# Kernel optimization log

Measured on AMD Instinct MI355X. Metric: run time of the kernel, lower is better.

The kernel has to match this reference:

```python
import jax, jax.numpy as jnp
import numpy as np

N_NODES = 50000
N_EDGES = 800000
IN_FEATS = 128
N_HIDDEN = 128
N_CLASSES = 64


def setup_inputs() -> dict:
    key = jax.random.key(0)
    ks = jax.random.split(key, 12)
    x = jax.random.normal(ks[0], (N_NODES, IN_FEATS), dtype=jnp.float32)
    src = jax.random.randint(ks[1], (N_EDGES,), 0, N_NODES, dtype=jnp.int32)
    dst = jax.random.randint(ks[2], (N_EDGES,), 0, N_NODES, dtype=jnp.int32)
    dims = [(IN_FEATS, N_HIDDEN), (N_HIDDEN, N_HIDDEN), (N_HIDDEN, N_CLASSES)]
    inp = {"x": x, "src": src, "dst": dst}
    for i, (din, dout) in enumerate(dims):
        s = (2.0 / (din + dout)) ** 0.5  # xavier-ish init scale
        inp[f"Wself{i}"] = jax.random.normal(ks[3 + 3 * i], (din, dout), dtype=jnp.float32) * s
        inp[f"Wneigh{i}"] = jax.random.normal(ks[4 + 3 * i], (din, dout), dtype=jnp.float32) * s
        inp[f"b{i}"] = jnp.zeros((dout,), dtype=jnp.float32)
    return inp


def _sage_conv(h, src, dst, inv_deg, Wself, Wneigh, b):
    # mean aggregation over in-neighbors: gather on src, segment-sum on dst
    agg = jax.ops.segment_sum(h[src], dst, num_segments=N_NODES)  # [N, d]
    h_neigh = agg * inv_deg[:, None]
    return h @ Wself + h_neigh @ Wneigh + b


def reference(x, src, dst, Wself0, Wneigh0, b0, Wself1, Wneigh1, b1, Wself2, Wneigh2, b2):
    # in-degree (clamped to 1, matching DGL mean aggregator), shared across layers
    deg = jax.ops.segment_sum(jnp.ones((N_EDGES,), dtype=jnp.float32), dst, num_segments=N_NODES)
    inv_deg = 1.0 / jnp.maximum(deg, 1.0)
    # dropout is identity in eval mode
    h = _sage_conv(x, src, dst, inv_deg, Wself0, Wneigh0, b0)
    h = jax.nn.relu(h)
    h = _sage_conv(h, src, dst, inv_deg, Wself1, Wneigh1, b1)
    h = jax.nn.relu(h)
    h = _sage_conv(h, src, dst, inv_deg, Wself2, Wneigh2, b2)
    return h
```

## Files before the change

kernel.cpp:

```cpp
#include <hip/hip_runtime.h>

#define N_NODES 50000
#define N_EDGES 800000
#define NB_SCAN 196

typedef unsigned short ushort_t;
typedef __attribute__((ext_vector_type(8))) short  short8v;
typedef __attribute__((ext_vector_type(4))) float  float4v;
typedef __attribute__((ext_vector_type(4))) unsigned short ushort4v;
typedef __attribute__((ext_vector_type(8))) unsigned short ushort8v;

__device__ __forceinline__ ushort_t f2bf(float f) {
    unsigned u = __float_as_uint(f);
    unsigned r = 0x7fffu + ((u >> 16) & 1u);
    return (ushort_t)((u + r) >> 16);
}
__device__ __forceinline__ float bf2f(ushort_t h) {
    return __uint_as_float((unsigned)h << 16);
}


__global__ void deg_count_k(const int* __restrict__ dst, int* __restrict__ deg, int nE) {
    int i = blockIdx.x * blockDim.x + threadIdx.x;
    if (i < nE) atomicAdd(deg + dst[i], 1);
}

__global__ __launch_bounds__(256) void block_sum_k(const int* __restrict__ deg,
                                                   int* __restrict__ bsum, int n) {
    __shared__ int s[256];
    int t = threadIdx.x, b = blockIdx.x;
    int i = b * 256 + t;
    s[t] = (i < n) ? deg[i] : 0;
    __syncthreads();
#pragma unroll
    for (int off = 128; off > 0; off >>= 1) {
        if (t < off) s[t] += s[t + off];
        __syncthreads();
    }
    if (t == 0) bsum[b] = s[0];
}

__global__ __launch_bounds__(256) void scan_bsum_k(const int* __restrict__ bsum,
                                                   int* __restrict__ boff,
                                                   int* __restrict__ rowptr_last, int nb) {
    __shared__ int s[256];
    int t = threadIdx.x;
    int v = (t < nb) ? bsum[t] : 0;
    s[t] = v;
    __syncthreads();
#pragma unroll
    for (int off = 1; off < 256; off <<= 1) {
        int u = (t >= off) ? s[t - off] : 0;
        __syncthreads();
        s[t] += u;
        __syncthreads();
    }
    if (t < nb) boff[t] = s[t] - v;
    if (t == 255) *rowptr_last = s[255];
}

__global__ __launch_bounds__(256) void write_rowptr_k(const int* __restrict__ deg,
                                                      const int* __restrict__ boff,
                                                      int* __restrict__ rowptr,
                                                      int* __restrict__ cursor,
                                                      float* __restrict__ inv, int n) {
    __shared__ int s[256];
    int t = threadIdx.x, b = blockIdx.x;
    int i = b * 256 + t;
    int d = (i < n) ? deg[i] : 0;
    s[t] = d;
    __syncthreads();
#pragma unroll
    for (int off = 1; off < 256; off <<= 1) {
        int u = (t >= off) ? s[t - off] : 0;
        __syncthreads();
        s[t] += u;
        __syncthreads();
    }
    if (i < n) {
        int r = boff[b] + s[t] - d;
        rowptr[i] = r;
        cursor[i] = r;
        inv[i] = 1.0f / fmaxf((float)d, 1.0f);
    }
}

__global__ __launch_bounds__(256) void scatter_k(const int* __restrict__ src,
                                                 const int* __restrict__ dst,
                                                 int* __restrict__ cursor,
                                                 int* __restrict__ csr, int nE) {
    const int grp = blockIdx.x & 7;
    const int lo = grp * 6250, hi = lo + 6250;
    const int stride = (gridDim.x >> 3) * 256;
    for (int i = (blockIdx.x >> 3) * 256 + threadIdx.x; i < nE; i += stride) {
        int d = dst[i];
        if (d >= lo && d < hi) {
            int s = src[i];
            int pos = atomicAdd(cursor + d, 1);
            csr[pos] = s;
        }
    }
}

__global__ __launch_bounds__(256) void cast_bf16_k(const float* __restrict__ x,
                                                   ushort_t* __restrict__ xb, int n4) {
    int i = blockIdx.x * 256 + threadIdx.x;
    if (i < n4) {
        float4 v = ((const float4*)x)[i];
        ushort4v h;
        h[0] = f2bf(v.x); h[1] = f2bf(v.y); h[2] = f2bf(v.z); h[3] = f2bf(v.w);
        ((ushort4v*)xb)[i] = h;
    }
}

__global__ __launch_bounds__(256) void pack_all_k(const float* __restrict__ W0n, const float* __restrict__ W0s,
                                                  const float* __restrict__ W1n, const float* __restrict__ W1s,
                                                  const float* __restrict__ W2n, const float* __restrict__ W2s,
                                                  ushort_t* __restrict__ P) {
    int tid = blockIdx.x * 256 + threadIdx.x;
    const float* W; int dout; int base; int r;
    if      (tid < 2048)  { W = W0n; dout = 128; base = 0;     r = tid; }
    else if (tid < 4096)  { W = W0s; dout = 128; base = 16384; r = tid - 2048; }
    else if (tid < 6144)  { W = W1n; dout = 128; base = 32768; r = tid - 4096; }
    else if (tid < 8192)  { W = W1s; dout = 128; base = 49152; r = tid - 6144; }
    else if (tid < 9216)  { W = W2n; dout = 64;  base = 65536; r = tid - 8192; }
    else                  { W = W2s; dout = 64;  base = 73728; r = tid - 9216; }
    int lane = r & 63;
    int ks = (r >> 6) & 3;
    int nt = r >> 8;
    int col = nt * 16 + (lane & 15);
    int k0 = ks * 32 + ((lane >> 4) << 3);
    ushort_t* d = P + (size_t)base + (size_t)r * 8;
    ushort4v lo4, hi4;
#pragma unroll
    for (int j = 0; j < 4; ++j) lo4[j] = f2bf(W[(size_t)(k0 + j) * dout + col]);
#pragma unroll
    for (int j = 0; j < 4; ++j) hi4[j] = f2bf(W[(size_t)(k0 + 4 + j) * dout + col]);
    *(ushort4v*)d = lo4;
    *(ushort4v*)(d + 4) = hi4;
}

__global__ __launch_bounds__(256) void aggm_k(const ushort_t* __restrict__ h,
                                              const int* __restrict__ rowptr,
                                              const int* __restrict__ csr,
                                              const float* __restrict__ inv,
                                              ushort_t* __restrict__ m, int N) {
    int node = (blockIdx.x * 256 + threadIdx.x) >> 5;
    int c = threadIdx.x & 31;
    if (node >= N) return;
    int start = rowptr[node], end = rowptr[node + 1];

    const ushort4v* hp = (const ushort4v*)h;
    float a0[4] = {}, a1[4] = {}, a2[4] = {}, a3[4] = {};
    int j = start;
    for (; j + 3 < end; j += 4) {
        int u0 = csr[j], u1 = csr[j + 1], u2 = csr[j + 2], u3 = csr[j + 3];
        ushort4v w0 = hp[(size_t)u0 * 32 + c];
        ushort4v w1 = hp[(size_t)u1 * 32 + c];
        ushort4v w2 = hp[(size_t)u2 * 32 + c];
        ushort4v w3 = hp[(size_t)u3 * 32 + c];
#pragma unroll
        for (int k = 0; k < 4; ++k) {
            a0[k] += bf2f(w0[k]); a1[k] += bf2f(w1[k]);
            a2[k] += bf2f(w2[k]); a3[k] += bf2f(w3[k]);
        }
    }
    for (; j < end; ++j) {
        ushort4v w = hp[(size_t)csr[j] * 32 + c];
#pragma unroll
        for (int k = 0; k < 4; ++k) a0[k] += bf2f(w[k]);
    }
    float s = inv[node];
    ushort4v o;
#pragma unroll
    for (int k = 0; k < 4; ++k) o[k] = f2bf(((a0[k] + a1[k]) + (a2[k] + a3[k])) * s);
    ((ushort4v*)m)[(size_t)node * 32 + c] = o;
}

__global__ __launch_bounds__(256, 2) void fusedgemm_k(const ushort_t* __restrict__ H,
                                                      const ushort_t* __restrict__ M,
                                                      const short8v* __restrict__ Ws,
                                                      const short8v* __restrict__ Wn,
                                                      const float* __restrict__ bias,
                                                      ushort_t* __restrict__ Out, int N) {
    __shared__ ushort_t sm[2][128 * 128];
    char* sbH = (char*)sm[0];
    char* sbM = (char*)sm[1];
    const int bm = blockIdx.x * 128;
    const int t = threadIdx.x;
    const int w = t >> 6, l = t & 63;

    {
        const ushort8v* Hp = (const ushort8v*)H;
        const ushort8v* Mp = (const ushort8v*)M;
        ushort8v zeroV = {0, 0, 0, 0, 0, 0, 0, 0};
#pragma unroll
        for (int it = 0; it < 8; ++it) {
            int r = it * 16 + (t >> 4);
            int row = bm + r;
            int byte = (r * 256 + (t & 15) * 16) ^ ((r & 7) << 4);
            ushort8v vh = zeroV, vm = zeroV;
            if (row < N) {
                vh = Hp[(size_t)row * 16 + (t & 15)];
                vm = Mp[(size_t)row * 16 + (t & 15)];
            }
            *(ushort8v*)(sbH + byte) = vh;
            *(ushort8v*)(sbM + byte) = vm;
        }
    }
    __syncthreads();

    float bv[8];
#pragma unroll
    for (int nt = 0; nt < 8; ++nt) bv[nt] = bias[nt * 16 + (l & 15)];

    float4v acc[2][8] = {};
#pragma unroll
    for (int ks = 0; ks < 4; ++ks) {
        int r0 = w * 32 + (l & 15);
        int r1 = r0 + 16;
        int b0 = (r0 * 256 + ks * 64 + (l >> 4) * 16) ^ ((r0 & 7) << 4);
        int b1 = (r1 * 256 + ks * 64 + (l >> 4) * 16) ^ ((r1 & 7) << 4);
        short8v ah0 = *(const short8v*)(sbH + b0);
        short8v ah1 = *(const short8v*)(sbH + b1);
        short8v am0 = *(const short8v*)(sbM + b0);
        short8v am1 = *(const short8v*)(sbM + b1);
#pragma unroll
        for (int nt = 0; nt < 8; ++nt) {
            short8v bs = Ws[(nt * 4 + ks) * 64 + l];
            short8v bn = Wn[(nt * 4 + ks) * 64 + l];
            acc[0][nt] = __builtin_amdgcn_mfma_f32_16x16x32_bf16(ah0, bs, acc[0][nt], 0, 0, 0);
            acc[0][nt] = __builtin_amdgcn_mfma_f32_16x16x32_bf16(am0, bn, acc[0][nt], 0, 0, 0);
            acc[1][nt] = __builtin_amdgcn_mfma_f32_16x16x32_bf16(ah1, bs, acc[1][nt], 0, 0, 0);
            acc[1][nt] = __builtin_amdgcn_mfma_f32_16x16x32_bf16(am1, bn, acc[1][nt], 0, 0, 0);
        }
    }

#pragma unroll
    for (int mi = 0; mi < 2; ++mi) {
#pragma unroll
        for (int i = 0; i < 4; ++i) {
            int row = bm + w * 32 + mi * 16 + (l >> 4) * 4 + i;
            if (row < N) {
#pragma unroll
                for (int nt = 0; nt < 8; ++nt) {
                    int col = nt * 16 + (l & 15);
                    Out[(size_t)row * 128 + col] = f2bf(fmaxf(acc[mi][nt][i] + bv[nt], 0.f));
                }
            }
        }
    }
}

__global__ __launch_bounds__(256, 2) void dual64_k(const ushort_t* __restrict__ A,
                                                   const short8v* __restrict__ Wn,
                                                   const short8v* __restrict__ Ws,
                                                   const float* __restrict__ bias,
                                                   ushort_t* __restrict__ Z,
                                                   float* __restrict__ S, int N) {
    constexpr int NT = 4;
    __shared__ ushort_t Asm[128 * 128];
    char* sb = (char*)Asm;
    const int bm = blockIdx.x * 128;
    const int t = threadIdx.x;
    const int w = t >> 6, l = t & 63;

    {
        const ushort8v* Ap = (const ushort8v*)A;
        ushort8v zeroV = {0, 0, 0, 0, 0, 0, 0, 0};
#pragma unroll
        for (int it = 0; it < 8; ++it) {
            int r = it * 16 + (t >> 4);
            int row = bm + r;
            ushort8v v = zeroV;
            if (row < N) v = Ap[(size_t)row * 16 + (t & 15)];
            int byte = (r * 256 + (t & 15) * 16) ^ ((r & 7) << 4);
            *(ushort8v*)(sb + byte) = v;
        }
    }
    __syncthreads();

    float bv[NT];
#pragma unroll
    for (int nt = 0; nt < NT; ++nt) bv[nt] = bias[nt * 16 + (l & 15)];

    float4v accS[2][NT] = {}, accN[2][NT] = {};
#pragma unroll
    for (int ks = 0; ks < 4; ++ks) {
        int r0 = w * 32 + (l & 15);
        int b0 = (r0 * 256 + ks * 64 + (l >> 4) * 16) ^ ((r0 & 7) << 4);
        short8v a0 = *(const short8v*)(sb + b0);
        int r1 = r0 + 16;
        int b1 = (r1 * 256 + ks * 64 + (l >> 4) * 16) ^ ((r1 & 7) << 4);
        short8v a1 = *(const short8v*)(sb + b1);
#pragma unroll
        for (int nt = 0; nt < NT; ++nt) {
            short8v bs = Ws[(nt * 4 + ks) * 64 + l];
            short8v bn = Wn[(nt * 4 + ks) * 64 + l];
            accS[0][nt] = __builtin_amdgcn_mfma_f32_16x16x32_bf16(a0, bs, accS[0][nt], 0, 0, 0);
            accS[1][nt] = __builtin_amdgcn_mfma_f32_16x16x32_bf16(a1, bs, accS[1][nt], 0, 0, 0);
            accN[0][nt] = __builtin_amdgcn_mfma_f32_16x16x32_bf16(a0, bn, accN[0][nt], 0, 0, 0);
            accN[1][nt] = __builtin_amdgcn_mfma_f32_16x16x32_bf16(a1, bn, accN[1][nt], 0, 0, 0);
        }
    }

#pragma unroll
    for (int mi = 0; mi < 2; ++mi) {
#pragma unroll
        for (int i = 0; i < 4; ++i) {
            int row = bm + w * 32 + mi * 16 + (l >> 4) * 4 + i;
            if (row < N) {
#pragma unroll
                for (int nt = 0; nt < NT; ++nt) {
                    int col = nt * 16 + (l & 15);
                    S[(size_t)row * 64 + col] = accS[mi][nt][i] + bv[nt];
                    Z[(size_t)row * 64 + col] = f2bf(accN[mi][nt][i]);
                }
            }
        }
    }
}

__global__ __launch_bounds__(256) void agg64_k(const ushort_t* __restrict__ z,
                                               const int* __restrict__ rowptr,
                                               const int* __restrict__ csr,
                                               const float* __restrict__ inv,
                                               float* __restrict__ out, int N) {
    int node = (blockIdx.x * 256 + threadIdx.x) >> 4;
    int c = threadIdx.x & 15;
    if (node >= N) return;
    int start = rowptr[node], end = rowptr[node + 1];

    const ushort4v* zp = (const ushort4v*)z;
    float a0[4] = {}, a1[4] = {}, a2[4] = {}, a3[4] = {};
    int j = start;
    for (; j + 3 < end; j += 4) {
        int u0 = csr[j], u1 = csr[j + 1], u2 = csr[j + 2], u3 = csr[j + 3];
        ushort4v w0 = zp[(size_t)u0 * 16 + c];
        ushort4v w1 = zp[(size_t)u1 * 16 + c];
        ushort4v w2 = zp[(size_t)u2 * 16 + c];
        ushort4v w3 = zp[(size_t)u3 * 16 + c];
#pragma unroll
        for (int k = 0; k < 4; ++k) {
            a0[k] += bf2f(w0[k]); a1[k] += bf2f(w1[k]);
            a2[k] += bf2f(w2[k]); a3[k] += bf2f(w3[k]);
        }
    }
    for (; j < end; ++j) {
        ushort4v w = zp[(size_t)csr[j] * 16 + c];
#pragma unroll
        for (int k = 0; k < 4; ++k) a0[k] += bf2f(w[k]);
    }
    float s = inv[node];
    float4* op = (float4*)(out + (size_t)node * 64 + c * 4);
    float4 o = *op;
    o.x += ((a0[0] + a1[0]) + (a2[0] + a3[0])) * s;
    o.y += ((a0[1] + a1[1]) + (a2[1] + a3[1])) * s;
    o.z += ((a0[2] + a1[2]) + (a2[2] + a3[2])) * s;
    o.w += ((a0[3] + a1[3]) + (a2[3] + a3[3])) * s;
    *op = o;
}


extern "C" void kernel_launch(void* const* d_in, const int* in_sizes, int n_in,
                              void* d_out, int out_size, void* d_ws, size_t ws_size,
                              hipStream_t stream) {
    const float* x       = (const float*)d_in[0];
    const int*   src     = (const int*)d_in[1];
    const int*   dst     = (const int*)d_in[2];
    const float* Wself0  = (const float*)d_in[3];
    const float* Wneigh0 = (const float*)d_in[4];
    const float* b0      = (const float*)d_in[5];
    const float* Wself1  = (const float*)d_in[6];
    const float* Wneigh1 = (const float*)d_in[7];
    const float* b1      = (const float*)d_in[8];
    const float* Wself2  = (const float*)d_in[9];
    const float* Wneigh2 = (const float*)d_in[10];
    const float* b2      = (const float*)d_in[11];
    float* out = (float*)d_out;

    char* ws = (char*)d_ws;
    size_t off = 0;
    auto alloc = [&](size_t bytes) -> void* {
        void* p = ws + off;
        off += (bytes + 255) & ~(size_t)255;
        return p;
    };
    int*      deg    = (int*)alloc((size_t)N_NODES * 4);
    float*    inv    = (float*)alloc((size_t)N_NODES * 4);
    int*      rowptr = (int*)alloc((size_t)(N_NODES + 1) * 4);
    int*      cursor = (int*)alloc((size_t)N_NODES * 4);
    int*      csr    = (int*)alloc((size_t)N_EDGES * 4);
    int*      bsum   = (int*)alloc((size_t)NB_SCAN * 4);
    int*      boff   = (int*)alloc((size_t)NB_SCAN * 4);
    ushort_t* packW  = (ushort_t*)alloc((size_t)81920 * 2);
    ushort_t* xb     = (ushort_t*)alloc((size_t)N_NODES * 128 * 2);
    ushort_t* mbuf   = (ushort_t*)alloc((size_t)N_NODES * 128 * 2);
    ushort_t* h1     = (ushort_t*)alloc((size_t)N_NODES * 128 * 2);
    ushort_t* h2     = (ushort_t*)alloc((size_t)N_NODES * 128 * 2);
    ushort_t* z64    = (ushort_t*)alloc((size_t)N_NODES * 64 * 2);

    dim3 b256(256);
    const int edgeBlocks  = (N_EDGES + 255) / 256;
    const int gemmBlocks  = (N_NODES + 127) / 128;
    const int aggmBlocks  = (N_NODES * 32 + 255) / 256;
    const int agg64Blocks = (N_NODES * 16 + 255) / 256;
    const int castBlocks  = (N_NODES * 128 / 4 + 255) / 256;

    hipMemsetAsync(deg, 0, (size_t)N_NODES * 4, stream);
    deg_count_k<<<edgeBlocks, b256, 0, stream>>>(dst, deg, N_EDGES);
    block_sum_k<<<NB_SCAN, b256, 0, stream>>>(deg, bsum, N_NODES);
    scan_bsum_k<<<1, b256, 0, stream>>>(bsum, boff, rowptr + N_NODES, NB_SCAN);
    write_rowptr_k<<<NB_SCAN, b256, 0, stream>>>(deg, boff, rowptr, cursor, inv, N_NODES);
    scatter_k<<<1024, b256, 0, stream>>>(src, dst, cursor, csr, N_EDGES);

    pack_all_k<<<40, b256, 0, stream>>>(Wneigh0, Wself0, Wneigh1, Wself1, Wneigh2, Wself2, packW);
    cast_bf16_k<<<castBlocks, b256, 0, stream>>>(x, xb, N_NODES * 128 / 4);
    const short8v* pN0 = (const short8v*)(packW);
    const short8v* pS0 = (const short8v*)(packW + 16384);
    const short8v* pN1 = (const short8v*)(packW + 32768);
    const short8v* pS1 = (const short8v*)(packW + 49152);
    const short8v* pN2 = (const short8v*)(packW + 65536);
    const short8v* pS2 = (const short8v*)(packW + 73728);

    aggm_k<<<aggmBlocks, b256, 0, stream>>>(xb, rowptr, csr, inv, mbuf, N_NODES);
    fusedgemm_k<<<gemmBlocks, b256, 0, stream>>>(xb, mbuf, pS0, pN0, b0, h1, N_NODES);

    aggm_k<<<aggmBlocks, b256, 0, stream>>>(h1, rowptr, csr, inv, mbuf, N_NODES);
    fusedgemm_k<<<gemmBlocks, b256, 0, stream>>>(h1, mbuf, pS1, pN1, b1, h2, N_NODES);

    dual64_k<<<gemmBlocks, b256, 0, stream>>>(h2, pN2, pS2, b2, z64, out, N_NODES);
    agg64_k<<<agg64Blocks, b256, 0, stream>>>(z64, rowptr, csr, inv, out, N_NODES);
}
```

Measured before the change: 225.3 us.

## Fuse CSR build and bf16 cast into one cooperative kernel; widen aggregation loads

Replaces the memset, degree count, three scan kernels, scatter and cast kernels with a single cooperative kernel that separates the phases with grid-wide syncs, removing several launches and the gaps between them. Separately, the aggregation kernels now load 8 bf16 values per thread (16-byte loads) instead of 4, halving the threads per node and doubling per-thread work. The grid syncs add barrier cost, and the 1024-block cooperative launch requires every block to be co-resident; if they cannot all be resident the launch fails and nothing downstream runs correctly.

Result: slower. 710.9 us (+215.6%).

```diff
diff --git a/kernel.cpp b/kernel.cpp
--- a/kernel.cpp
+++ b/kernel.cpp
@@ -1,4 +1,7 @@
 #include <hip/hip_runtime.h>
+#include <hip/hip_cooperative_groups.h>
+
+namespace cg = cooperative_groups;
 
 #define N_NODES 50000
 #define N_EDGES 800000
@@ -20,96 +23,96 @@
 }
 
 
-__global__ void deg_count_k(const int* __restrict__ dst, int* __restrict__ deg, int nE) {
-    int i = blockIdx.x * blockDim.x + threadIdx.x;
-    if (i < nE) atomicAdd(deg + dst[i], 1);
-}
-
-__global__ __launch_bounds__(256) void block_sum_k(const int* __restrict__ deg,
-                                                   int* __restrict__ bsum, int n) {
+__global__ __launch_bounds__(256) void build_k(const float* __restrict__ x,
+                                               ushort_t* __restrict__ xb,
+                                               const int* __restrict__ src,
+                                               const int* __restrict__ dst,
+                                               int* __restrict__ deg,
+                                               float* __restrict__ inv,
+                                               int* __restrict__ rowptr,
+                                               int* __restrict__ cursor,
+                                               int* __restrict__ csr,
+                                               int* __restrict__ bsum) {
+    cg::grid_group grid = cg::this_grid();
     __shared__ int s[256];
-    int t = threadIdx.x, b = blockIdx.x;
-    int i = b * 256 + t;
-    s[t] = (i < n) ? deg[i] : 0;
-    __syncthreads();
-#pragma unroll
-    for (int off = 128; off > 0; off >>= 1) {
-        if (t < off) s[t] += s[t + off];
-        __syncthreads();
-    }
-    if (t == 0) bsum[b] = s[0];
-}
-
-__global__ __launch_bounds__(256) void scan_bsum_k(const int* __restrict__ bsum,
-                                                   int* __restrict__ boff,
-                                                   int* __restrict__ rowptr_last, int nb) {
-    __shared__ int s[256];
-    int t = threadIdx.x;
-    int v = (t < nb) ? bsum[t] : 0;
-    s[t] = v;
-    __syncthreads();
-#pragma unroll
-    for (int off = 1; off < 256; off <<= 1) {
-        int u = (t >= off) ? s[t - off] : 0;
-        __syncthreads();
-        s[t] += u;
-        __syncthreads();
-    }
-    if (t < nb) boff[t] = s[t] - v;
-    if (t == 255) *rowptr_last = s[255];
-}
-
-__global__ __launch_bounds__(256) void write_rowptr_k(const int* __restrict__ deg,
-                                                      const int* __restrict__ boff,
-                                                      int* __restrict__ rowptr,
-                                                      int* __restrict__ cursor,
-                                                      float* __restrict__ inv, int n) {
-    __shared__ int s[256];
-    int t = threadIdx.x, b = blockIdx.x;
-    int i = b * 256 + t;
-    int d = (i < n) ? deg[i] : 0;
-    s[t] = d;
-    __syncthreads();
-#pragma unroll
-    for (int off = 1; off < 256; off <<= 1) {
-        int u = (t >= off) ? s[t - off] : 0;
-        __syncthreads();
-        s[t] += u;
-        __syncthreads();
-    }
-    if (i < n) {
-        int r = boff[b] + s[t] - d;
-        rowptr[i] = r;
-        cursor[i] = r;
-        inv[i] = 1.0f / fmaxf((float)d, 1.0f);
-    }
-}
-
-__global__ __launch_bounds__(256) void scatter_k(const int* __restrict__ src,
-                                                 const int* __restrict__ dst,
-                                                 int* __restrict__ cursor,
-                                                 int* __restrict__ csr, int nE) {
-    const int grp = blockIdx.x & 7;
-    const int lo = grp * 6250, hi = lo + 6250;
-    const int stride = (gridDim.x >> 3) * 256;
-    for (int i = (blockIdx.x >> 3) * 256 + threadIdx.x; i < nE; i += stride) {
-        int d = dst[i];
-        if (d >= lo && d < hi) {
-            int s = src[i];
-            int pos = atomicAdd(cursor + d, 1);
-            csr[pos] = s;
-        }
-    }
-}
-
-__global__ __launch_bounds__(256) void cast_bf16_k(const float* __restrict__ x,
-                                                   ushort_t* __restrict__ xb, int n4) {
-    int i = blockIdx.x * 256 + threadIdx.x;
-    if (i < n4) {
+    const int t = threadIdx.x, b = blockIdx.x;
+    const int nthr = gridDim.x * 256;
+    const int gtid = b * 256 + t;
+
+    for (int i = gtid; i < N_NODES; i += nthr) deg[i] = 0;
+    for (int i = gtid; i < N_NODES * 32; i += nthr) {
         float4 v = ((const float4*)x)[i];
         ushort4v h;
         h[0] = f2bf(v.x); h[1] = f2bf(v.y); h[2] = f2bf(v.z); h[3] = f2bf(v.w);
         ((ushort4v*)xb)[i] = h;
+    }
+    grid.sync();
+
+    for (int i = gtid; i < N_EDGES; i += nthr) atomicAdd(deg + dst[i], 1);
+    grid.sync();
+
+    if (b < NB_SCAN) {
+        int i = b * 256 + t;
+        s[t] = (i < N_NODES) ? deg[i] : 0;
+        __syncthreads();
+#pragma unroll
+        for (int off = 128; off > 0; off >>= 1) {
+            if (t < off) s[t] += s[t + off];
+            __syncthreads();
+        }
+        if (t == 0) bsum[b] = s[0];
+    }
+    grid.sync();
+
+    if (b == 0) {
+        int v = (t < NB_SCAN) ? bsum[t] : 0;
+        s[t] = v;
+        __syncthreads();
+#pragma unroll
+        for (int off = 1; off < 256; off <<= 1) {
+            int u = (t >= off) ? s[t - off] : 0;
+            __syncthreads();
+            s[t] += u;
+            __syncthreads();
+        }
+        if (t < NB_SCAN) bsum[t] = s[t] - v;
+        if (t == 255) rowptr[N_NODES] = s[255];
+    }
+    grid.sync();
+
+    if (b < NB_SCAN) {
+        int i = b * 256 + t;
+        int d = (i < N_NODES) ? deg[i] : 0;
+        s[t] = d;
+        __syncthreads();
+#pragma unroll
+        for (int off = 1; off < 256; off <<= 1) {
+            int u = (t >= off) ? s[t - off] : 0;
+            __syncthreads();
+            s[t] += u;
+            __syncthreads();
+        }
+        if (i < N_NODES) {
+            int r = bsum[b] + s[t] - d;
+            rowptr[i] = r;
+            cursor[i] = r;
+            inv[i] = 1.0f / fmaxf((float)d, 1.0f);
+        }
+    }
+    grid.sync();
+
+    {
+        const int grp = b & 7;
+        const int lo = grp * 6250, hi = lo + 6250;
+        const int stride = (gridDim.x >> 3) * 256;
+        for (int i = (b >> 3) * 256 + t; i < N_EDGES; i += stride) {
+            int d = dst[i];
+            if (d >= lo && d < hi) {
+                int sv = src[i];
+                int pos = atomicAdd(cursor + d, 1);
+                csr[pos] = sv;
+            }
+        }
     }
 }
 
@@ -145,36 +148,36 @@
                                               const int* __restrict__ csr,
                                               const float* __restrict__ inv,
                                               ushort_t* __restrict__ m, int N) {
-    int node = (blockIdx.x * 256 + threadIdx.x) >> 5;
-    int c = threadIdx.x & 31;
+    int node = (blockIdx.x * 256 + threadIdx.x) >> 4;
+    int c = threadIdx.x & 15;
     if (node >= N) return;
     int start = rowptr[node], end = rowptr[node + 1];
 
-    const ushort4v* hp = (const ushort4v*)h;
-    float a0[4] = {}, a1[4] = {}, a2[4] = {}, a3[4] = {};
+    const ushort8v* hp = (const ushort8v*)h;
+    float a0[8] = {}, a1[8] = {}, a2[8] = {}, a3[8] = {};
     int j = start;
     for (; j + 3 < end; j += 4) {
         int u0 = csr[j], u1 = csr[j + 1], u2 = csr[j + 2], u3 = csr[j + 3];
-        ushort4v w0 = hp[(size_t)u0 * 32 + c];
-        ushort4v w1 = hp[(size_t)u1 * 32 + c];
-        ushort4v w2 = hp[(size_t)u2 * 32 + c];
-        ushort4v w3 = hp[(size_t)u3 * 32 + c];
-#pragma unroll
-        for (int k = 0; k < 4; ++k) {
+        ushort8v w0 = hp[(size_t)u0 * 16 + c];
+        ushort8v w1 = hp[(size_t)u1 * 16 + c];
+        ushort8v w2 = hp[(size_t)u2 * 16 + c];
+        ushort8v w3 = hp[(size_t)u3 * 16 + c];
+#pragma unroll
+        for (int k = 0; k < 8; ++k) {
             a0[k] += bf2f(w0[k]); a1[k] += bf2f(w1[k]);
             a2[k] += bf2f(w2[k]); a3[k] += bf2f(w3[k]);
         }
     }
     for (; j < end; ++j) {
-        ushort4v w = hp[(size_t)csr[j] * 32 + c];
-#pragma unroll
-        for (int k = 0; k < 4; ++k) a0[k] += bf2f(w[k]);
+        ushort8v w = hp[(size_t)csr[j] * 16 + c];
+#pragma unroll
+        for (int k = 0; k < 8; ++k) a0[k] += bf2f(w[k]);
     }
     float s = inv[node];
-    ushort4v o;
-#pragma unroll
-    for (int k = 0; k < 4; ++k) o[k] = f2bf(((a0[k] + a1[k]) + (a2[k] + a3[k])) * s);
-    ((ushort4v*)m)[(size_t)node * 32 + c] = o;
+    ushort8v o;
+#pragma unroll
+    for (int k = 0; k < 8; ++k) o[k] = f2bf(((a0[k] + a1[k]) + (a2[k] + a3[k])) * s);
+    ((ushort8v*)m)[(size_t)node * 16 + c] = o;
 }
 
 __global__ __launch_bounds__(256, 2) void fusedgemm_k(const ushort_t* __restrict__ H,
@@ -326,39 +329,45 @@
                                                const int* __restrict__ csr,
                                                const float* __restrict__ inv,
                                                float* __restrict__ out, int N) {
-    int node = (blockIdx.x * 256 + threadIdx.x) >> 4;
-    int c = threadIdx.x & 15;
+    int node = (blockIdx.x * 256 + threadIdx.x) >> 3;
+    int c = threadIdx.x & 7;
     if (node >= N) return;
     int start = rowptr[node], end = rowptr[node + 1];
 
-    const ushort4v* zp = (const ushort4v*)z;
-    float a0[4] = {}, a1[4] = {}, a2[4] = {}, a3[4] = {};
+    const ushort8v* zp = (const ushort8v*)z;
+    float a0[8] = {}, a1[8] = {}, a2[8] = {}, a3[8] = {};
     int j = start;
     for (; j + 3 < end; j += 4) {
         int u0 = csr[j], u1 = csr[j + 1], u2 = csr[j + 2], u3 = csr[j + 3];
-        ushort4v w0 = zp[(size_t)u0 * 16 + c];
-        ushort4v w1 = zp[(size_t)u1 * 16 + c];
-        ushort4v w2 = zp[(size_t)u2 * 16 + c];
-        ushort4v w3 = zp[(size_t)u3 * 16 + c];
-#pragma unroll
-        for (int k = 0; k < 4; ++k) {
+        ushort8v w0 = zp[(size_t)u0 * 8 + c];
+        ushort8v w1 = zp[(size_t)u1 * 8 + c];
+        ushort8v w2 = zp[(size_t)u2 * 8 + c];
+        ushort8v w3 = zp[(size_t)u3 * 8 + c];
+#pragma unroll
+        for (int k = 0; k < 8; ++k) {
             a0[k] += bf2f(w0[k]); a1[k] += bf2f(w1[k]);
             a2[k] += bf2f(w2[k]); a3[k] += bf2f(w3[k]);
         }
     }
     for (; j < end; ++j) {
-        ushort4v w = zp[(size_t)csr[j] * 16 + c];
-#pragma unroll
-        for (int k = 0; k < 4; ++k) a0[k] += bf2f(w[k]);
+        ushort8v w = zp[(size_t)csr[j] * 8 + c];
+#pragma unroll
+        for (int k = 0; k < 8; ++k) a0[k] += bf2f(w[k]);
     }
     float s = inv[node];
-    float4* op = (float4*)(out + (size_t)node * 64 + c * 4);
-    float4 o = *op;
-    o.x += ((a0[0] + a1[0]) + (a2[0] + a3[0])) * s;
-    o.y += ((a0[1] + a1[1]) + (a2[1] + a3[1])) * s;
-    o.z += ((a0[2] + a1[2]) + (a2[2] + a3[2])) * s;
-    o.w += ((a0[3] + a1[3]) + (a2[3] + a3[3])) * s;
-    *op = o;
+    float* op = out + (size_t)node * 64 + c * 8;
+    float4 o0 = *(float4*)op;
+    float4 o1 = *(float4*)(op + 4);
+    o0.x += ((a0[0] + a1[0]) + (a2[0] + a3[0])) * s;
+    o0.y += ((a0[1] + a1[1]) + (a2[1] + a3[1])) * s;
+    o0.z += ((a0[2] + a1[2]) + (a2[2] + a3[2])) * s;
+    o0.w += ((a0[3] + a1[3]) + (a2[3] + a3[3])) * s;
+    o1.x += ((a0[4] + a1[4]) + (a2[4] + a3[4])) * s;
+    o1.y += ((a0[5] + a1[5]) + (a2[5] + a3[5])) * s;
+    o1.z += ((a0[6] + a1[6]) + (a2[6] + a3[6])) * s;
+    o1.w += ((a0[7] + a1[7]) + (a2[7] + a3[7])) * s;
+    *(float4*)op = o0;
+    *(float4*)(op + 4) = o1;
 }
 
 
@@ -392,7 +401,6 @@
     int*      cursor = (int*)alloc((size_t)N_NODES * 4);
     int*      csr    = (int*)alloc((size_t)N_EDGES * 4);
     int*      bsum   = (int*)alloc((size_t)NB_SCAN * 4);
-    int*      boff   = (int*)alloc((size_t)NB_SCAN * 4);
     ushort_t* packW  = (ushort_t*)alloc((size_t)81920 * 2);
     ushort_t* xb     = (ushort_t*)alloc((size_t)N_NODES * 128 * 2);
     ushort_t* mbuf   = (ushort_t*)alloc((size_t)N_NODES * 128 * 2);
@@ -401,21 +409,19 @@
     ushort_t* z64    = (ushort_t*)alloc((size_t)N_NODES * 64 * 2);
 
     dim3 b256(256);
-    const int edgeBlocks  = (N_EDGES + 255) / 256;
     const int gemmBlocks  = (N_NODES + 127) / 128;
-    const int aggmBlocks  = (N_NODES * 32 + 255) / 256;
-    const int agg64Blocks = (N_NODES * 16 + 255) / 256;
-    const int castBlocks  = (N_NODES * 128 / 4 + 255) / 256;
-
-    hipMemsetAsync(deg, 0, (size_t)N_NODES * 4, stream);
-    deg_count_k<<<edgeBlocks, b256, 0, stream>>>(dst, deg, N_EDGES);
-    block_sum_k<<<NB_SCAN, b256, 0, stream>>>(deg, bsum, N_NODES);
-    scan_bsum_k<<<1, b256, 0, stream>>>(bsum, boff, rowptr + N_NODES, NB_SCAN);
-    write_rowptr_k<<<NB_SCAN, b256, 0, stream>>>(deg, boff, rowptr, cursor, inv, N_NODES);
-    scatter_k<<<1024, b256, 0, stream>>>(src, dst, cursor, csr, N_EDGES);
+    const int aggmBlocks  = (N_NODES * 16 + 255) / 256;
+    const int agg64Blocks = (N_NODES * 8 + 255) / 256;
+
+    {
+        void* args[] = {(void*)&x, (void*)&xb, (void*)&src, (void*)&dst,
+                        (void*)&deg, (void*)&inv, (void*)&rowptr, (void*)&cursor,
+                        (void*)&csr, (void*)&bsum};
+        hipLaunchCooperativeKernel(reinterpret_cast<const void*>(build_k),
+                                   dim3(1024), b256, args, 0, stream);
+    }
 
     pack_all_k<<<40, b256, 0, stream>>>(Wneigh0, Wself0, Wneigh1, Wself1, Wneigh2, Wself2, packW);
-    cast_bf16_k<<<castBlocks, b256, 0, stream>>>(x, xb, N_NODES * 128 / 4);
     const short8v* pN0 = (const short8v*)(packW);
     const short8v* pS0 = (const short8v*)(packW + 16384);
     const short8v* pN1 = (const short8v*)(packW + 32768);
```
